# Kernel tuning notes

Measured on AMD Instinct MI355X. Metric: run time of the kernel, lower is better.

Reference implementation:

```python
import jax, jax.numpy as jnp
import numpy as np

B, T, D, H, KVH, HD, L, V, FF = 8, 512, 1024, 16, 4, 64, 4, 32000, 4096
ROPE_BASE = 10000.0


def _layernorm(x, g, b):
    m = jnp.mean(x, axis=-1, keepdims=True)
    v = jnp.var(x, axis=-1, keepdims=True)
    return (x - m) * jax.lax.rsqrt(v + 1e-5) * g + b


def setup_inputs() -> dict:
    key = jax.random.key(0)
    ks = jax.random.split(key, 8)
    s = 0.02
    kv = KVH * HD
    return {
        "input_ids": jax.random.randint(ks[0], (B, T), 0, V),
        "wte": jax.random.normal(ks[1], (V, D), jnp.float32) * s,
        "ln1_g": jnp.ones((L, D), jnp.float32),
        "ln1_b": jnp.zeros((L, D), jnp.float32),
        "c_attn_w": jax.random.normal(ks[2], (L, D, H * HD + 2 * kv), jnp.float32) * s,
        "c_attn_b": jnp.zeros((L, H * HD + 2 * kv), jnp.float32),
        "c_proj_w": jax.random.normal(ks[3], (L, D, D), jnp.float32) * s,
        "c_proj_b": jnp.zeros((L, D), jnp.float32),
        "ln2_g": jnp.ones((L, D), jnp.float32),
        "ln2_b": jnp.zeros((L, D), jnp.float32),
        "fc_w": jax.random.normal(ks[4], (L, D, FF), jnp.float32) * s,
        "fc_b": jnp.zeros((L, FF), jnp.float32),
        "proj_w": jax.random.normal(ks[5], (L, FF, D), jnp.float32) * s,
        "proj_b": jnp.zeros((L, D), jnp.float32),
        "lnf_g": jnp.ones((D,), jnp.float32),
        "lnf_b": jnp.zeros((D,), jnp.float32),
        "lm_w": jax.random.normal(ks[6], (D, V), jnp.float32) * s,
    }


def _forward(input_ids, wte, ln1_g, ln1_b, c_attn_w, c_attn_b, c_proj_w, c_proj_b,
             ln2_g, ln2_b, fc_w, fc_b, proj_w, proj_b, lnf_g, lnf_b, lm_w):
    x = wte[input_ids]  # [B, T, D]

    # Precomputed rotary frequencies (freqs_cos / freqs_sin buffers)
    t = jnp.arange(T, dtype=jnp.float32)
    inv = 1.0 / (ROPE_BASE ** (jnp.arange(0, HD, 2, dtype=jnp.float32) / HD))
    ang = t[:, None] * inv[None, :]  # [T, HD//2]
    cos, sin = jnp.cos(ang), jnp.sin(ang)
    causal = jnp.tril(jnp.ones((T, T), bool))

    def rope(u):  # u: [B, h, T, HD], even/odd interleave
        ue, uo = u[..., 0::2], u[..., 1::2]
        re = ue * cos - uo * sin
        ro = ue * sin + uo * cos
        return jnp.stack([re, ro], axis=-1).reshape(u.shape)

    def block(x, p):
        l1g, l1b, aw, ab, pw, pb, l2g, l2b, fw, fb, ow, ob = p
        h = _layernorm(x, l1g, l1b)
        qkv = h @ aw + ab  # [B, T, H*HD + 2*KVH*HD]
        q, k, v = jnp.split(qkv, [H * HD, H * HD + KVH * HD], axis=-1)
        q = q.reshape(B, T, H, HD).transpose(0, 2, 1, 3)
        k = k.reshape(B, T, KVH, HD).transpose(0, 2, 1, 3)
        v = v.reshape(B, T, KVH, HD).transpose(0, 2, 1, 3)
        rep = H // KVH
        k = jnp.repeat(k, rep, axis=1)  # GQA repeat_interleave
        v = jnp.repeat(v, rep, axis=1)
        q, k = rope(q), rope(k)
        att = jnp.einsum('bhqd,bhkd->bhqk', q, k) * (1.0 / jnp.sqrt(jnp.float32(HD)))
        att = jnp.where(causal, att, -jnp.inf)
        att = jax.nn.softmax(att, axis=-1)
        y = jnp.einsum('bhqk,bhkd->bhqd', att, v)
        y = y.transpose(0, 2, 1, 3).reshape(B, T, D)
        x = x + (y @ pw + pb)
        h2 = _layernorm(x, l2g, l2b)
        m = jax.nn.gelu(h2 @ fw + fb, approximate=False)
        x = x + (m @ ow + ob)
        return x, None

    xs = (ln1_g, ln1_b, c_attn_w, c_attn_b, c_proj_w, c_proj_b,
          ln2_g, ln2_b, fc_w, fc_b, proj_w, proj_b)
    x, _ = jax.lax.scan(block, x, xs)
    x = _layernorm(x, lnf_g, lnf_b)
    return x @ lm_w  # [B, T, V]


def reference(input_ids, wte, ln1_g, ln1_b, c_attn_w, c_attn_b, c_proj_w, c_proj_b,
              ln2_g, ln2_b, fc_w, fc_b, proj_w, proj_b, lnf_g, lnf_b, lm_w):
    return _forward(input_ids, wte, ln1_g, ln1_b, c_attn_w, c_attn_b, c_proj_w,
                    c_proj_b, ln2_g, ln2_b, fc_w, fc_b, proj_w, proj_b,
                    lnf_g, lnf_b, lm_w)
```

## Files before the change

### kernel.cpp

```cpp
#include <hip/hip_runtime.h>
#include <math.h>

typedef unsigned short u16;
typedef unsigned int   u32;
typedef __bf16  bf16x8 __attribute__((ext_vector_type(8)));
typedef float   f32x4  __attribute__((ext_vector_type(4)));

#define Bz   8
#define Tz   512
#define Dz   1024
#define Hz   16
#define KVHz 4
#define HDz  64
#define Lz   4
#define Vz   32000
#define FFz  4096
#define Mz   (Bz*Tz)
#define QKVz (Hz*HDz + 2*KVHz*HDz)

__device__ __forceinline__ u16 bf16r(float f) {
    u32 u = __builtin_bit_cast(u32, f);
    u += 0x7fffu + ((u >> 16) & 1u);
    return (u16)(u >> 16);
}
__device__ __forceinline__ float b2f(u16 u) {
    u32 v = ((u32)u) << 16;
    return __builtin_bit_cast(float, v);
}
__device__ __forceinline__ float fast_erf(float x) {
    const float ax = fabsf(x);
    const float t  = 1.f / (1.f + 0.3275911f * ax);
    const float y  = t * (0.254829592f + t * (-0.284496736f + t * (1.421413741f +
                     t * (-1.453152027f + t * 1.061405429f))));
    const float r  = 1.f - y * __expf(-ax * ax);
    return copysignf(r, x);
}
__device__ __forceinline__ void glds16(const void* g, void* l) {
    __builtin_amdgcn_global_load_lds(
        (__attribute__((address_space(1))) unsigned int*)(unsigned long long)g,
        (__attribute__((address_space(3))) unsigned int*)l, 16, 0, 0);
}

__global__ __launch_bounds__(256) void embed_kernel(const int* __restrict__ ids,
                                                    const float* __restrict__ wte,
                                                    float* __restrict__ x) {
    const int row = blockIdx.x;
    const int id  = ids[row];
    ((float4*)(x + (size_t)row * Dz))[threadIdx.x] =
        ((const float4*)(wte + (size_t)id * Dz))[threadIdx.x];
}

__global__ __launch_bounds__(256) void transpose_cvt_kernel(const float* __restrict__ in,
                                                            u16* __restrict__ out,
                                                            int K, int N) {
    __shared__ float tile[64][65];
    const size_t lofs = (size_t)blockIdx.z * (size_t)K * (size_t)N;
    const float* inp = in + lofs;
    u16* outp = out + lofs;
    const int nt = blockIdx.x << 6, kt = blockIdx.y << 6;
    const int c4 = (threadIdx.x & 15) << 2;
    const int r0 = threadIdx.x >> 4;
#pragma unroll
    for (int rr = 0; rr < 64; rr += 16) {
        const int r = rr + r0;
        float4 v = *(const float4*)(inp + (size_t)(kt + r) * N + nt + c4);
        tile[r][c4] = v.x; tile[r][c4 + 1] = v.y; tile[r][c4 + 2] = v.z; tile[r][c4 + 3] = v.w;
    }
    __syncthreads();
    const int n0 = threadIdx.x >> 2;
    const int kk = (threadIdx.x & 3) << 4;
    u16* ob = outp + (size_t)(nt + n0) * K + kt + kk;
#pragma unroll
    for (int g = 0; g < 4; ++g) {
        ushort4 uo;
        uo.x = bf16r(tile[kk + g * 4 + 0][n0]);
        uo.y = bf16r(tile[kk + g * 4 + 1][n0]);
        uo.z = bf16r(tile[kk + g * 4 + 2][n0]);
        uo.w = bf16r(tile[kk + g * 4 + 3][n0]);
        *(ushort4*)(ob + g * 4) = uo;
    }
}

__global__ __launch_bounds__(256) void ln_kernel(const float* __restrict__ x,
                                                 const float* __restrict__ g,
                                                 const float* __restrict__ bb,
                                                 u16* __restrict__ out) {
    const int row = blockIdx.x;
    const float4 v = ((const float4*)(x + (size_t)row * Dz))[threadIdx.x];
    float s = v.x + v.y + v.z + v.w;
    float q = v.x * v.x + v.y * v.y + v.z * v.z + v.w * v.w;
#pragma unroll
    for (int m = 32; m > 0; m >>= 1) { s += __shfl_xor(s, m, 64); q += __shfl_xor(q, m, 64); }
    __shared__ float ss[4], qq[4];
    const int wid = threadIdx.x >> 6, lane = threadIdx.x & 63;
    if (lane == 0) { ss[wid] = s; qq[wid] = q; }
    __syncthreads();
    s = ss[0] + ss[1] + ss[2] + ss[3];
    q = qq[0] + qq[1] + qq[2] + qq[3];
    const float mean = s * (1.f / 1024.f);
    const float rstd = rsqrtf(q * (1.f / 1024.f) - mean * mean + 1e-5f);
    const float4 gv = ((const float4*)g)[threadIdx.x];
    const float4 bv = ((const float4*)bb)[threadIdx.x];
    ushort4 o;
    o.x = bf16r((v.x - mean) * rstd * gv.x + bv.x);
    o.y = bf16r((v.y - mean) * rstd * gv.y + bv.y);
    o.z = bf16r((v.z - mean) * rstd * gv.z + bv.z);
    o.w = bf16r((v.w - mean) * rstd * gv.w + bv.w);
    ((ushort4*)(out + (size_t)row * Dz))[threadIdx.x] = o;
}

__global__ __launch_bounds__(256) void rope_split_kernel(const float* __restrict__ qkv,
                                                         u16* __restrict__ q,
                                                         u16* __restrict__ k,
                                                         u16* __restrict__ vt) {
    const int row = blockIdx.x;
    const int b = row >> 9, t = row & 511;
    const float* src = qkv + (size_t)row * QKVz;
    const float ft = (float)t;
    for (int p = threadIdx.x; p < 512; p += 256) {
        const int h = p >> 5, i = p & 31;
        const float e = src[h * 64 + 2 * i], o = src[h * 64 + 2 * i + 1];
        const float ang = ft * exp2f((float)i * -0.41524101186092029f);
        float sn, cs; sincosf(ang, &sn, &cs);
        const size_t qi = (size_t)((b * 16 + h) * 512 + t) * 64 + 2 * i;
        q[qi]     = bf16r((e * cs - o * sn) * 0.125f);
        q[qi + 1] = bf16r((e * sn + o * cs) * 0.125f);
    }
    for (int p = threadIdx.x; p < 128; p += 256) {
        const int h = p >> 5, i = p & 31;
        const float e = src[1024 + h * 64 + 2 * i], o = src[1024 + h * 64 + 2 * i + 1];
        const float ang = ft * exp2f((float)i * -0.41524101186092029f);
        float sn, cs; sincosf(ang, &sn, &cs);
        const size_t ki = (size_t)((b * 4 + h) * 512 + t) * 64 + 2 * i;
        k[ki]     = bf16r(e * cs - o * sn);
        k[ki + 1] = bf16r(e * sn + o * cs);
    }
    for (int p = threadIdx.x; p < 128; p += 256) {
        const int h = p >> 5, i = p & 31;
        const float e = src[1280 + 2 * p], o = src[1280 + 2 * p + 1];
        const size_t vbase = (size_t)(b * 4 + h) * (64 * 512);
        vt[vbase + (size_t)(2 * i)     * 512 + t] = bf16r(e);
        vt[vbase + (size_t)(2 * i + 1) * 512 + t] = bf16r(o);
    }
}

__global__ __launch_bounds__(256) void attn_kernel(const u16* __restrict__ q,
                                                   const u16* __restrict__ k,
                                                   const u16* __restrict__ vt,
                                                   u16* __restrict__ y) {
    __shared__ __align__(16) u16 plds[4][16 * 40];
    const int tid = threadIdx.x;
    const int w = tid >> 6, lane = tid & 63;
    const int l15 = lane & 15, g = lane >> 4;

    const int bid = blockIdx.x;
    const int qt = bid & 7, h = (bid >> 3) & 15, b = bid >> 7;
    const int kvh = h >> 2;
    const int q0 = qt * 64 + w * 16;
    const u16* qbase  = q  + ((size_t)(b * 16 + h)  * 512 + q0) * 64;
    const u16* kbase  = k  + (size_t)(b * 4 + kvh) * (512 * 64);
    const u16* vtbase = vt + (size_t)(b * 4 + kvh) * (64 * 512);

    const bf16x8 qf0 = *(const bf16x8*)(qbase + (size_t)l15 * 64 + g * 8);
    const bf16x8 qf1 = *(const bf16x8*)(qbase + (size_t)l15 * 64 + 32 + g * 8);

    f32x4 so[4];
#pragma unroll
    for (int dt = 0; dt < 4; ++dt) so[dt] = (f32x4){0.f, 0.f, 0.f, 0.f};
    float m[4]    = {-1e30f, -1e30f, -1e30f, -1e30f};
    float lsum[4] = {0.f, 0.f, 0.f, 0.f};
    const int qrow = q0 + g * 4;
    u16* pw = &plds[w][0];

    const int nch = ((q0 + 15) >> 5) + 1;
    for (int c = 0; c < nch; ++c) {
        const int kc = c << 5;
        const u16* kp = kbase + (size_t)(kc + l15) * 64 + g * 8;
        const bf16x8 kl0 = *(const bf16x8*)(kp);
        const bf16x8 kl1 = *(const bf16x8*)(kp + 32);
        const bf16x8 kh0 = *(const bf16x8*)(kp + 16 * 64);
        const bf16x8 kh1 = *(const bf16x8*)(kp + 16 * 64 + 32);
        f32x4 slo = (f32x4){0.f, 0.f, 0.f, 0.f};
        f32x4 shi = (f32x4){0.f, 0.f, 0.f, 0.f};
        slo = __builtin_amdgcn_mfma_f32_16x16x32_bf16(qf0, kl0, slo, 0, 0, 0);
        slo = __builtin_amdgcn_mfma_f32_16x16x32_bf16(qf1, kl1, slo, 0, 0, 0);
        shi = __builtin_amdgcn_mfma_f32_16x16x32_bf16(qf0, kh0, shi, 0, 0, 0);
        shi = __builtin_amdgcn_mfma_f32_16x16x32_bf16(qf1, kh1, shi, 0, 0, 0);
        bf16x8 vf[4];
#pragma unroll
        for (int dt = 0; dt < 4; ++dt)
            vf[dt] = *(const bf16x8*)(vtbase + (size_t)(dt * 16 + l15) * 512 + kc + g * 8);
        const int kvlo = kc + l15, kvhi = kvlo + 16;
#pragma unroll
        for (int r = 0; r < 4; ++r) {
            const int qg = qrow + r;
            if (kvlo > qg) slo[r] = -1e30f;
            if (kvhi > qg) shi[r] = -1e30f;
        }
        float pe0[4], pe1[4], alpha[4];
#pragma unroll
        for (int r = 0; r < 4; ++r) {
            float t = fmaxf(slo[r], shi[r]);
#pragma unroll
            for (int mm = 8; mm > 0; mm >>= 1) t = fmaxf(t, __shfl_xor(t, mm, 64));
            const float mnew = fmaxf(m[r], t);
            pe0[r] = __expf(slo[r] - mnew);
            pe1[r] = __expf(shi[r] - mnew);
            float cs = pe0[r] + pe1[r];
#pragma unroll
            for (int mm = 8; mm > 0; mm >>= 1) cs += __shfl_xor(cs, mm, 64);
            alpha[r] = __expf(m[r] - mnew);
            lsum[r] = lsum[r] * alpha[r] + cs;
            m[r] = mnew;
        }
#pragma unroll
        for (int dt = 0; dt < 4; ++dt)
#pragma unroll
            for (int r = 0; r < 4; ++r) so[dt][r] *= alpha[r];
#pragma unroll
        for (int r = 0; r < 4; ++r) {
            pw[(g * 4 + r) * 40 + l15]      = bf16r(pe0[r]);
            pw[(g * 4 + r) * 40 + 16 + l15] = bf16r(pe1[r]);
        }
        asm volatile("s_waitcnt lgkmcnt(0)" ::: "memory");
        __builtin_amdgcn_sched_barrier(0);
        const bf16x8 pf = *(const bf16x8*)(pw + l15 * 40 + g * 8);
#pragma unroll
        for (int dt = 0; dt < 4; ++dt)
            so[dt] = __builtin_amdgcn_mfma_f32_16x16x32_bf16(pf, vf[dt], so[dt], 0, 0, 0);
        asm volatile("" ::: "memory");
    }
#pragma unroll
    for (int dt = 0; dt < 4; ++dt) {
#pragma unroll
        for (int r = 0; r < 4; ++r) {
            const int qg = qrow + r;
            y[(size_t)(b * 512 + qg) * 1024 + h * 64 + dt * 16 + l15] =
                bf16r(so[dt][r] / lsum[r]);
        }
    }
}

template <int EPI>
__global__ __launch_bounds__(256) void gemm_kernel(const u16* __restrict__ A,
                                                   const u16* __restrict__ Bt,
                                                   const float* __restrict__ bias,
                                                   const float* __restrict__ resid,
                                                   float* __restrict__ outF,
                                                   u16* __restrict__ outU,
                                                   int N, int K) {
    __shared__ __align__(16) u16 lA[3][4096];
    __shared__ __align__(16) u16 lB[3][4096];
    const int tid = threadIdx.x;
    const int wid = tid >> 6, lane = tid & 63;

    const int ntx = gridDim.x;
    const int bid = blockIdx.y * ntx + blockIdx.x;
    const int gsz = ntx << 3;
    const int g   = bid / gsz;
    const int rem = bid - g * gsz;
    const int m0 = ((g << 3) + (rem & 7)) << 7;
    const int n0 = (rem >> 3) << 7;

    const int wm = (wid >> 1) << 6, wn = (wid & 1) << 6;
    const int kc = lane >> 4, l15 = lane & 15;

    const u16* gA = A  + (size_t)(m0 + (tid & 127)) * K + ((tid >> 7) << 3);
    const u16* gB = Bt + (size_t)(n0 + (tid & 127)) * K + ((tid >> 7) << 3);
    const int wofs = wid << 9;

    f32x4 acc[4][4];
#pragma unroll
    for (int i = 0; i < 4; ++i)
#pragma unroll
        for (int j = 0; j < 4; ++j) acc[i][j] = (f32x4){0.f, 0.f, 0.f, 0.f};

    auto stage = [&](int c) {
        glds16(gA, &lA[c][wofs]); glds16(gA + 16, &lA[c][2048 + wofs]);
        glds16(gB, &lB[c][wofs]); glds16(gB + 16, &lB[c][2048 + wofs]);
        gA += 32; gB += 32;
    };
    auto compute = [&](int c) {
        const bf16x8* lAv = (const bf16x8*)lA[c];
        const bf16x8* lBv = (const bf16x8*)lB[c];
        bf16x8 af[4], bfr[4];
#pragma unroll
        for (int tt = 0; tt < 4; ++tt) {
            af[tt]  = lAv[kc * 128 + wm + tt * 16 + l15];
            bfr[tt] = lBv[kc * 128 + wn + tt * 16 + l15];
        }
        __builtin_amdgcn_s_setprio(1);
#pragma unroll
        for (int tm = 0; tm < 4; ++tm)
#pragma unroll
            for (int tn = 0; tn < 4; ++tn)
                acc[tm][tn] = __builtin_amdgcn_mfma_f32_16x16x32_bf16(af[tm], bfr[tn],
                                                                      acc[tm][tn], 0, 0, 0);
        __builtin_amdgcn_s_setprio(0);
    };

    const int nk = K >> 5;
    stage(0); stage(1);

    int cb = 0, sb = 2;
    for (int t = 0; t < nk - 1; ++t) {
        asm volatile("s_waitcnt vmcnt(4)" ::: "memory");
        __builtin_amdgcn_s_barrier();
        if (t + 2 < nk) stage(sb);
        compute(cb);
        cb = (cb == 2) ? 0 : cb + 1;
        sb = (sb == 2) ? 0 : sb + 1;
    }
    asm volatile("s_waitcnt vmcnt(0)" ::: "memory");
    __builtin_amdgcn_s_barrier();
    compute(cb);

    const int rbase = (lane >> 4) << 2;
#pragma unroll
    for (int tn = 0; tn < 4; ++tn) {
        const int gc = n0 + wn + tn * 16 + l15;
        float bv = 0.f;
        if (EPI != 3) bv = bias[gc];
#pragma unroll
        for (int tm = 0; tm < 4; ++tm) {
#pragma unroll
            for (int r = 0; r < 4; ++r) {
                const int gr = m0 + wm + tm * 16 + rbase + r;
                const size_t idx = (size_t)gr * N + gc;
                float vv = acc[tm][tn][r] + bv;
                if (EPI == 1) vv += resid[idx];
                if (EPI == 2) {
                    const float gl = 0.5f * vv * (1.f + fast_erf(vv * 0.70710678118654752f));
                    outU[idx] = bf16r(gl);
                } else {
                    outF[idx] = vv;
                }
            }
        }
    }
}

#define PHASE2(c, kh, STAGE)                                                   \
  {                                                                            \
    bf16x8 af[8], bfr[4];                                                      \
    _Pragma("unroll") for (int j = 0; j < 8; ++j)                              \
      af[j] = smv[(c) * 4096 + (kh) * 512 + aoff + j * 16];                    \
    _Pragma("unroll") for (int n = 0; n < 4; ++n)                              \
      bfr[n] = smv[(c) * 4096 + (kh) * 512 + boff + n * 16];                   \
    STAGE;                                                                     \
    __builtin_amdgcn_s_barrier();                                              \
    asm volatile("s_waitcnt lgkmcnt(0)" ::: "memory");                         \
    __builtin_amdgcn_s_setprio(1);                                             \
    _Pragma("unroll") for (int j = 0; j < 8; ++j)                              \
      _Pragma("unroll") for (int n = 0; n < 4; ++n)                            \
        acc[j][n] = __builtin_amdgcn_mfma_f32_16x16x32_bf16(                   \
            af[j], bfr[n], acc[j][n], 0, 0, 0);                                \
    __builtin_amdgcn_s_setprio(0);                                             \
    asm volatile("s_waitcnt vmcnt(8)" ::: "memory");                           \
    __builtin_amdgcn_s_barrier();                                              \
  }

template <int EPI>
__global__ __launch_bounds__(512) void gemm256_kernel(const u16* __restrict__ A,
                                                      const u16* __restrict__ Bt,
                                                      const float* __restrict__ bias,
                                                      float* __restrict__ outF,
                                                      u16* __restrict__ outU,
                                                      int N, int K) {
    const int NTt = N >> 8;
    const int bid = blockIdx.x;
    const int xcd = bid & 7;
    const int window = bid >> 8;
    const int pos = (bid >> 3) & 31;
    const int strip = xcd & 3;
    const int scol = (xcd >> 2) + (window << 1);
    const int mt = (strip << 2) + (pos & 3);
    const int nt = (scol << 3) + (pos >> 2);
    if (nt >= NTt) return;
    const int m0 = mt << 8, n0 = nt << 8;

    __shared__ __align__(16) u16 sm[65536];
    const int tid = threadIdx.x;
    const int wid = tid >> 6, lane = tid & 63;
    const int wr = wid >> 2, wc = wid & 3;
    const int kc = lane >> 4, l15 = lane & 15;

    const int s_kc  = wid >> 1;
    const int s_row = ((wid & 1) << 6) + lane;
    const int s_u   = wid << 6;

    const u16* gA0 = A  + (size_t)(m0 + s_row) * K + s_kc * 8;
    const u16* gA1 = gA0 + (size_t)128 * K;
    const u16* gB0 = Bt + (size_t)(n0 + s_row) * K + s_kc * 8;
    const u16* gB1 = gB0 + (size_t)128 * K;

    f32x4 acc[8][4];
#pragma unroll
    for (int i = 0; i < 8; ++i)
#pragma unroll
        for (int j = 0; j < 4; ++j) acc[i][j] = (f32x4){0.f, 0.f, 0.f, 0.f};

    const bf16x8* smv = (const bf16x8*)sm;
    const int aoff = wr * 1024 + kc * 128 + l15;
    const int boff = 2048 + (wc >> 1) * 1024 + kc * 128 + ((wc & 1) << 6) + l15;

    auto stA = [&](int kt, int kh, int c) {
        const int ko = kt * 64 + kh * 32;
        const int ub = c * 4096 + kh * 512 + s_u;
        glds16(gA0 + ko, &sm[(size_t)ub * 8]);
        glds16(gA1 + ko, &sm[(size_t)(ub + 1024) * 8]);
    };
    auto stB = [&](int kt, int kh, int c) {
        const int ko = kt * 64 + kh * 32;
        const int ub = 2048 + c * 4096 + kh * 512 + s_u;
        glds16(gB0 + ko, &sm[(size_t)ub * 8]);
        glds16(gB1 + ko, &sm[(size_t)(ub + 1024) * 8]);
    };

    const int nk = K >> 6;
    stA(0, 0, 0); stB(0, 0, 0);
    stA(0, 1, 0); stB(0, 1, 0);
    stA(1, 0, 1); stB(1, 0, 1);
    asm volatile("s_waitcnt vmcnt(4)" ::: "memory");
    __builtin_amdgcn_s_barrier();

    const int niter = nk >> 1;
    for (int i = 0; i < niter; ++i) {
        const int t1 = 2 * i + 1;
        const int t2 = (2 * i + 2 < nk) ? 2 * i + 2 : nk - 1;
        const int t3 = (2 * i + 3 < nk) ? 2 * i + 3 : nk - 1;
        PHASE2(0, 0, { stA(t1, 1, 1); stB(t1, 1, 1); })
        PHASE2(0, 1, { stA(t2, 0, 0); stB(t2, 0, 0); })
        PHASE2(1, 0, { stA(t2, 1, 0); stB(t2, 1, 0); })
        PHASE2(1, 1, { stA(t3, 0, 1); stB(t3, 0, 1); })
    }
    asm volatile("s_waitcnt vmcnt(0)" ::: "memory");

    const int rbase = (lane >> 4) << 2;
#pragma unroll
    for (int n = 0; n < 4; ++n) {
        const int gc = n0 + wc * 64 + n * 16 + l15;
        float bv = 0.f;
        if (EPI == 2) bv = bias[gc];
#pragma unroll
        for (int f = 0; f < 8; ++f) {
#pragma unroll
            for (int r = 0; r < 4; ++r) {
                const int gr = m0 + wr * 128 + f * 16 + rbase + r;
                const size_t idx = (size_t)gr * N + gc;
                float vv = acc[f][n][r] + bv;
                if (EPI == 2) {
                    const float gl = 0.5f * vv * (1.f + fast_erf(vv * 0.70710678118654752f));
                    outU[idx] = bf16r(gl);
                } else {
                    outF[idx] = vv;
                }
            }
        }
    }
}

extern "C" void kernel_launch(void* const* d_in, const int* in_sizes, int n_in,
                              void* d_out, int out_size, void* d_ws, size_t ws_size,
                              hipStream_t stream) {
    const int*   ids      = (const int*)d_in[0];
    const float* wte      = (const float*)d_in[1];
    const float* ln1_g    = (const float*)d_in[2];
    const float* ln1_b    = (const float*)d_in[3];
    const float* c_attn_w = (const float*)d_in[4];
    const float* c_attn_b = (const float*)d_in[5];
    const float* c_proj_w = (const float*)d_in[6];
    const float* c_proj_b = (const float*)d_in[7];
    const float* ln2_g    = (const float*)d_in[8];
    const float* ln2_b    = (const float*)d_in[9];
    const float* fc_w     = (const float*)d_in[10];
    const float* fc_b     = (const float*)d_in[11];
    const float* proj_w   = (const float*)d_in[12];
    const float* proj_b   = (const float*)d_in[13];
    const float* lnf_g    = (const float*)d_in[14];
    const float* lnf_b    = (const float*)d_in[15];
    const float* lm_w     = (const float*)d_in[16];
    float* out = (float*)d_out;

    char* w = (char*)d_ws;
    auto take = [&](size_t bytes) { void* p = (void*)w; w += (bytes + 255) & ~(size_t)255; return p; };
    u16*   wqkvT = (u16*)take((size_t)Lz * QKVz * Dz * 2);
    u16*   wprojT= (u16*)take((size_t)Lz * Dz * Dz * 2);
    u16*   wfcT  = (u16*)take((size_t)Lz * FFz * Dz * 2);
    u16*   wmlpT = (u16*)take((size_t)Lz * Dz * FFz * 2);
    u16*   wlmT  = (u16*)take((size_t)Vz * Dz * 2);
    float* x     = (float*)take((size_t)Mz * Dz * 4);
    u16*   h     = (u16*)take((size_t)Mz * Dz * 2);
    float* qkv   = (float*)take((size_t)Mz * QKVz * 4);
    u16*   qb    = (u16*)take((size_t)Mz * Dz * 2);
    u16*   kb    = (u16*)take((size_t)Bz * KVHz * Tz * HDz * 2);
    u16*   vb    = (u16*)take((size_t)Bz * KVHz * Tz * HDz * 2);
    u16*   yb    = (u16*)take((size_t)Mz * Dz * 2);
    u16*   mb    = (u16*)take((size_t)Mz * FFz * 2);
    (void)ws_size; (void)in_sizes; (void)n_in; (void)out_size;

    const dim3 tb(256);
    transpose_cvt_kernel<<<dim3(QKVz / 64, Dz / 64, Lz), tb, 0, stream>>>(c_attn_w, wqkvT, Dz, QKVz);
    transpose_cvt_kernel<<<dim3(Dz / 64, Dz / 64, Lz), tb, 0, stream>>>(c_proj_w, wprojT, Dz, Dz);
    transpose_cvt_kernel<<<dim3(FFz / 64, Dz / 64, Lz), tb, 0, stream>>>(fc_w, wfcT, Dz, FFz);
    transpose_cvt_kernel<<<dim3(Dz / 64, FFz / 64, Lz), tb, 0, stream>>>(proj_w, wmlpT, FFz, Dz);
    transpose_cvt_kernel<<<dim3(Vz / 64, Dz / 64, 1), tb, 0, stream>>>(lm_w, wlmT, Dz, Vz);

    embed_kernel<<<Mz, tb, 0, stream>>>(ids, wte, x);

    const int fc_grid = 128 * (((FFz / 256) + 7) / 8);
    const int lm_grid = 128 * (((Vz / 256) + 7) / 8);

    for (int l = 0; l < Lz; ++l) {
        ln_kernel<<<Mz, tb, 0, stream>>>(x, ln1_g + l * Dz, ln1_b + l * Dz, h);
        gemm_kernel<0><<<dim3(QKVz / 128, Mz / 128), tb, 0, stream>>>(
            h, wqkvT + (size_t)l * QKVz * Dz, c_attn_b + l * QKVz, nullptr, qkv, nullptr, QKVz, Dz);
        rope_split_kernel<<<Mz, tb, 0, stream>>>(qkv, qb, kb, vb);
        attn_kernel<<<Bz * Hz * (Tz / 64), tb, 0, stream>>>(qb, kb, vb, yb);
        gemm_kernel<1><<<dim3(Dz / 128, Mz / 128), tb, 0, stream>>>(
            yb, wprojT + (size_t)l * Dz * Dz, c_proj_b + l * Dz, x, x, nullptr, Dz, Dz);
        ln_kernel<<<Mz, tb, 0, stream>>>(x, ln2_g + l * Dz, ln2_b + l * Dz, h);
        gemm256_kernel<2><<<dim3(fc_grid), dim3(512), 0, stream>>>(
            h, wfcT + (size_t)l * FFz * Dz, fc_b + l * FFz, nullptr, mb, FFz, Dz);
        gemm_kernel<1><<<dim3(Dz / 128, Mz / 128), tb, 0, stream>>>(
            mb, wmlpT + (size_t)l * Dz * FFz, proj_b + l * Dz, x, x, nullptr, Dz, FFz);
    }
    ln_kernel<<<Mz, tb, 0, stream>>>(x, lnf_g, lnf_b, h);
    gemm256_kernel<3><<<dim3(lm_grid), dim3(512), 0, stream>>>(
        h, wlmT, nullptr, out, nullptr, Vz, Dz);
}
```

Before: 2.003 ms.

## Use a 256x128-tile double-buffered GEMM kernel for the LM head

Adds gemm_k2_kernel, a 512-thread GEMM with 256x128 output tiles, a K step of 32, two LDS buffers and global-to-LDS prefetch two stages ahead. It also raises MFMA priority around the inner loop. The LM-head projection now uses this kernel with a grid over 16 M tiles times 250 N tiles. The aim is to fix the poor tiling of the 32000-wide vocab dimension (32000 is not a multiple of 256) and to raise occupancy through smaller LDS use and launch_bounds(512,4). In exchange, each tile reuses data less than the 256x256 kernel did.

```diff
diff --git a/kernel.cpp b/kernel.cpp
--- a/kernel.cpp
+++ b/kernel.cpp
@@ -449,6 +449,98 @@
                 const int gr = m0 + wr * 128 + f * 16 + rbase + r;
                 const size_t idx = (size_t)gr * N + gc;
                 float vv = acc[f][n][r] + bv;
+                if (EPI == 2) {
+                    const float gl = 0.5f * vv * (1.f + fast_erf(vv * 0.70710678118654752f));
+                    outU[idx] = bf16r(gl);
+                } else {
+                    outF[idx] = vv;
+                }
+            }
+        }
+    }
+}
+
+template <int EPI>
+__global__ __launch_bounds__(512, 4) void gemm_k2_kernel(const u16* __restrict__ A,
+                                                         const u16* __restrict__ Bt,
+                                                         const float* __restrict__ bias,
+                                                         float* __restrict__ outF,
+                                                         u16* __restrict__ outU,
+                                                         int N, int K) {
+    __shared__ __align__(16) u16 sm[2][12288];
+    const int tid = threadIdx.x;
+    const int wid = tid >> 6, lane = tid & 63;
+    const int wr = wid >> 1, wc = wid & 1;
+    const int kcl = lane >> 4, l15 = lane & 15;
+
+    const int bid = blockIdx.x;
+    const int m0 = (bid & 15) << 8;
+    const int n0 = (bid >> 4) << 7;
+
+    const u16* gA = A  + (size_t)(m0 + ((wid & 3) << 6) + lane) * K + ((wid >> 2) << 3);
+    const u16* gB = Bt + (size_t)(n0 + ((wid & 1) << 6) + lane) * K + ((wid >> 1) << 3);
+    const int widu = wid << 9;
+
+    f32x4 acc[4][4];
+#pragma unroll
+    for (int i = 0; i < 4; ++i)
+#pragma unroll
+        for (int j = 0; j < 4; ++j) acc[i][j] = (f32x4){0.f, 0.f, 0.f, 0.f};
+
+    const bf16x8* smv = (const bf16x8*)sm;
+    const int abase = kcl * 256 + wr * 64 + l15;
+    const int bbase = 1024 + kcl * 128 + wc * 64 + l15;
+
+    auto stage = [&](int kt, int c) {
+        const int ko = kt << 5;
+        glds16(gA + ko,      &sm[c][widu]);
+        glds16(gA + ko + 16, &sm[c][4096 + widu]);
+        glds16(gB + ko,      &sm[c][8192 + widu]);
+    };
+
+    const int nk = K >> 5;
+    stage(0, 0); stage(1, 1);
+    asm volatile("s_waitcnt vmcnt(3)" ::: "memory");
+    __builtin_amdgcn_s_barrier();
+
+    int cur = 0;
+    for (int t = 0; t < nk; ++t) {
+        bf16x8 af[4], bf[4];
+#pragma unroll
+        for (int j = 0; j < 4; ++j) af[j] = smv[cur * 1536 + abase + j * 16];
+#pragma unroll
+        for (int n = 0; n < 4; ++n) bf[n] = smv[cur * 1536 + bbase + n * 16];
+        asm volatile("s_waitcnt lgkmcnt(0)" ::: "memory");
+        __builtin_amdgcn_s_barrier();
+        const bool pre = (t + 2 < nk);
+        if (pre) stage(t + 2, cur);
+        __builtin_amdgcn_s_setprio(1);
+#pragma unroll
+        for (int j = 0; j < 4; ++j)
+#pragma unroll
+            for (int n = 0; n < 4; ++n)
+                acc[j][n] = __builtin_amdgcn_mfma_f32_16x16x32_bf16(af[j], bf[n],
+                                                                    acc[j][n], 0, 0, 0);
+        __builtin_amdgcn_s_setprio(0);
+        if (pre) { asm volatile("s_waitcnt vmcnt(3)" ::: "memory"); }
+        else     { asm volatile("s_waitcnt vmcnt(0)" ::: "memory"); }
+        __builtin_amdgcn_s_barrier();
+        cur ^= 1;
+    }
+
+    const int rbase = kcl << 2;
+#pragma unroll
+    for (int n = 0; n < 4; ++n) {
+        const int gc = n0 + wc * 64 + n * 16 + l15;
+        float bv = 0.f;
+        if (EPI == 2) bv = bias[gc];
+#pragma unroll
+        for (int j = 0; j < 4; ++j) {
+#pragma unroll
+            for (int r = 0; r < 4; ++r) {
+                const int gr = m0 + wr * 64 + j * 16 + rbase + r;
+                const size_t idx = (size_t)gr * N + gc;
+                float vv = acc[j][n][r] + bv;
                 if (EPI == 2) {
                     const float gl = 0.5f * vv * (1.f + fast_erf(vv * 0.70710678118654752f));
                     outU[idx] = bf16r(gl);
@@ -509,7 +601,7 @@
     embed_kernel<<<Mz, tb, 0, stream>>>(ids, wte, x);
 
     const int fc_grid = 128 * (((FFz / 256) + 7) / 8);
-    const int lm_grid = 128 * (((Vz / 256) + 7) / 8);
+    const int lm_grid = (Mz / 256) * (Vz / 128);
 
     for (int l = 0; l < Lz; ++l) {
         ln_kernel<<<Mz, tb, 0, stream>>>(x, ln1_g + l * Dz, ln1_b + l * Dz, h);
@@ -526,6 +618,6 @@
             mb, wmlpT + (size_t)l * Dz * FFz, proj_b + l * Dz, x, x, nullptr, Dz, FFz);
     }
     ln_kernel<<<Mz, tb, 0, stream>>>(x, lnf_g, lnf_b, h);
-    gemm256_kernel<3><<<dim3(lm_grid), dim3(512), 0, stream>>>(
+    gemm_k2_kernel<3><<<dim3(lm_grid), dim3(512), 0, stream>>>(
         h, wlmT, nullptr, out, nullptr, Vz, Dz);
 }
```

Result: slower. 2.083 ms (+4.0%).
